# Performance work log

Hardware: AMD Instinct MI355X
Metric: run time of the kernel (lower is better)

The kernel has to match this reference:

```python
import jax, jax.numpy as jnp
import numpy as np

N_POINTS = 200000   # number of voxels
N_CLUSTS = 4096     # number of clusters
P = 64              # points per cluster (regularized fixed size)
E = 32768           # number of (directed) edges


def setup_inputs() -> dict:
    key = jax.random.key(0)
    k1, k2, k3 = jax.random.split(key, 3)
    data = jax.random.normal(k1, (N_POINTS, 4), dtype=jnp.float32)
    clusts = jax.random.randint(k2, (N_CLUSTS, P), 0, N_POINTS, dtype=jnp.int64)
    edge_index = jax.random.randint(k3, (2, E), 0, N_CLUSTS, dtype=jnp.int64)
    return {"data": data, "clusts": clusts, "edge_index": edge_index}


def reference(data, clusts, edge_index):
    coords = data[:, 1:4]                      # [N, 3] voxel coordinates
    c1 = clusts[edge_index[0]]                 # [E, P] point indices of source cluster
    c2 = clusts[edge_index[1]]                 # [E, P] point indices of target cluster
    x1 = coords[c1]                            # [E, P, 3]
    x2 = coords[c2]                            # [E, P, 3]
    e, p = c1.shape
    # pairwise squared distances per edge: [E, P, P]
    d2 = jnp.sum((x1[:, :, None, :] - x2[:, None, :, :]) ** 2, axis=-1)
    imin = jnp.argmin(d2.reshape(e, p * p), axis=1)   # flat argmin of closest pair
    i1 = imin // p
    i2 = imin % p
    v1 = jnp.take_along_axis(x1, i1[:, None, None], axis=1)[:, 0, :]  # [E, 3]
    v2 = jnp.take_along_axis(x2, i2[:, None, None], axis=1)[:, 0, :]  # [E, 3]
    disp = v1 - v2                                                    # [E, 3]
    lend = jnp.linalg.norm(disp, axis=1, keepdims=True)               # [E, 1]
    safe = jnp.where(lend > 0, lend, jnp.ones_like(lend))
    disp = jnp.where(lend > 0, disp / safe, disp)                     # unit displacement
    B = (disp[:, :, None] * disp[:, None, :]).reshape(e, 9)           # outer product, flat
    return jnp.concatenate([v1, v2, disp, lend, B], axis=1)           # [E, 19]
```

## Files before the change

### kernel.cpp

```cpp
#include <hip/hip_runtime.h>

#ifndef FLT_MAX
#define FLT_MAX 3.402823466e+38f
#endif

typedef float v2f __attribute__((ext_vector_type(2)));
typedef float v4f __attribute__((ext_vector_type(4)));
typedef float sf8 __attribute__((ext_vector_type(8)));

__device__ __forceinline__ float rlanef(float v, int l) {
    return __uint_as_float(__builtin_amdgcn_readlane(__float_as_uint(v), l));
}

__device__ __forceinline__ float sel3(int i, float a, float b, float c) {
    return i == 0 ? a : (i == 1 ? b : c);
}

__device__ __forceinline__ float sel4(int i, float a, float b, float c, float d) {
    return i == 0 ? a : (i == 1 ? b : (i == 2 ? c : d));
}

__device__ __forceinline__ float d2f(float ax, float ay, float az,
                                     float bx, float by, float bz) {
    const float dx = __fsub_rn(ax, bx);
    const float dy = __fsub_rn(ay, by);
    const float dz = __fsub_rn(az, bz);
    return __builtin_fmaf(dx, dx, __builtin_fmaf(dy, dy, __fmul_rn(dz, dz)));
}

__device__ __forceinline__ v2f d2p(v2f ax, v2f ay, v2f az, v2f bx, v2f by, v2f bz) {
    const v2f dx = ax - bx, dy = ay - by, dz = az - bz;
    return __builtin_elementwise_fma(dx, dx,
           __builtin_elementwise_fma(dy, dy, dz * dz));
}

__global__ __launch_bounds__(256) void build_table_kernel(
    const float* __restrict__ data,
    const int*   __restrict__ clusts,
    float*       __restrict__ T,
    int C)
{
    const int c = blockIdx.x * 4 + (threadIdx.x >> 6);
    const int p = threadIdx.x & 63;
    if (c >= C) return;
    const int pid = clusts[c * 64 + p];
    const float4 d = *reinterpret_cast<const float4*>(data + (size_t)pid * 4);
    float* row = T + (size_t)c * 192;
    row[p]       = d.y;
    row[p + 64]  = d.z;
    row[p + 128] = d.w;
}

__global__ __launch_bounds__(256) void clustgeo_sload_kernel(
    const float* __restrict__ T,
    const int*   __restrict__ eidx,
    float*       __restrict__ out,
    int E)
{
    const int wave = threadIdx.x >> 6;
    const int lane = threadIdx.x & 63;
    const int e = blockIdx.x * 4 + wave;
    const int ec = e < E ? e : (E - 1);

    const int ca = __builtin_amdgcn_readfirstlane(eidx[ec]);
    const int cb = __builtin_amdgcn_readfirstlane(eidx[E + ec]);
    const float* ta = T + (size_t)ca * 192;
    const float* tb = T + (size_t)cb * 192;

    const float rx = ta[lane];
    const float ry = ta[64 + lane];
    const float rz = ta[128 + lane];
    const v2f rxx = {rx, rx}, ryy = {ry, ry}, rzz = {rz, rz};

    v2f a01 = {FLT_MAX, FLT_MAX};
    v2f a23 = {FLT_MAX, FLT_MAX};

#define COLPAIR(XS, YS, ZS, U, ACC) do {                                       \
    const v2f cx = __builtin_shufflevector(XS, XS, 2*(U), 2*(U)+1);            \
    const v2f cy = __builtin_shufflevector(YS, YS, 2*(U), 2*(U)+1);            \
    const v2f cz = __builtin_shufflevector(ZS, ZS, 2*(U), 2*(U)+1);            \
    ACC = __builtin_elementwise_min(ACC, d2p(rxx, ryy, rzz, cx, cy, cz));      \
} while (0)

#define CHUNK(K) do {                                                          \
    sf8 Xs, Ys, Zs;                                                            \
    asm volatile("s_load_dwordx8 %0, %3, %4\n\t"                               \
                 "s_load_dwordx8 %1, %3, %5\n\t"                               \
                 "s_load_dwordx8 %2, %3, %6\n\t"                               \
                 "s_waitcnt lgkmcnt(0)"                                        \
                 : "=&s"(Xs), "=&s"(Ys), "=&s"(Zs)                             \
                 : "s"(tb), "n"((K) * 32), "n"(256 + (K) * 32),                \
                   "n"(512 + (K) * 32));                                       \
    COLPAIR(Xs, Ys, Zs, 0, a01);                                               \
    COLPAIR(Xs, Ys, Zs, 1, a23);                                               \
    COLPAIR(Xs, Ys, Zs, 2, a01);                                               \
    COLPAIR(Xs, Ys, Zs, 3, a23);                                               \
} while (0)

    CHUNK(0); CHUNK(1); CHUNK(2); CHUNK(3);
    CHUNK(4); CHUNK(5); CHUNK(6); CHUNK(7);
#undef CHUNK
#undef COLPAIR

    const float rowmin = fminf(fminf(a01.x, a01.y), fminf(a23.x, a23.y));

    float bm = rowmin;
    #pragma unroll
    for (int off = 32; off; off >>= 1) bm = fminf(bm, __shfl_xor(bm, off, 64));

    const unsigned long long mi = __ballot(rowmin == bm);
    const int i1 = (int)__ffsll(mi) - 1;
    const float v1x = rlanef(rx, i1);
    const float v1y = rlanef(ry, i1);
    const float v1z = rlanef(rz, i1);

    const float cx2 = tb[lane];
    const float cy2 = tb[64 + lane];
    const float cz2 = tb[128 + lane];
    const float dj = d2f(v1x, v1y, v1z, cx2, cy2, cz2);
    const unsigned long long mj = __ballot(dj == bm);
    const int i2 = (int)__ffsll(mj) - 1;
    const float v2x = rlanef(cx2, i2);
    const float v2y = rlanef(cy2, i2);
    const float v2z = rlanef(cz2, i2);

    float dx = v1x - v2x, dy = v1y - v2y, dz = v1z - v2z;
    const float lend = sqrtf(dx * dx + dy * dy + dz * dz);
    if (lend > 0.f) { dx /= lend; dy /= lend; dz /= lend; }

    if (lane < 19 && e < E) {
        float o;
        if (lane < 3)       o = sel3(lane,     v1x, v1y, v1z);
        else if (lane < 6)  o = sel3(lane - 3, v2x, v2y, v2z);
        else if (lane < 9)  o = sel3(lane - 6, dx, dy, dz);
        else if (lane == 9) o = lend;
        else {
            const int k = lane - 10;
            o = sel3(k / 3, dx, dy, dz) * sel3(k % 3, dx, dy, dz);
        }
        out[(size_t)e * 19 + lane] = o;
    }
}

#define SLICE 196
__global__ __launch_bounds__(256, 4) void clustgeo_edge_fallback(
    const float* __restrict__ data,
    const int*   __restrict__ clusts,
    const int*   __restrict__ eidx,
    float*       __restrict__ out,
    int E)
{
    const int wave = threadIdx.x >> 6;
    const int lane = threadIdx.x & 63;
    const int t    = lane & 15;
    const int gsh  = lane & 48;
    const int e    = blockIdx.x * 16 + wave * 4 + (lane >> 4);
    const int ec   = e < E ? e : (E - 1);

    __shared__ __align__(16) float sx[4][4][SLICE];

    const int ca = eidx[ec];
    const int cb = eidx[E + ec];
    const int4 P1 = *reinterpret_cast<const int4*>(clusts + ca * 64 + 4 * t);
    const int4 P2 = *reinterpret_cast<const int4*>(clusts + cb * 64 + 4 * t);
    const float4 q10 = *reinterpret_cast<const float4*>(data + (size_t)P1.x * 4);
    const float4 q11 = *reinterpret_cast<const float4*>(data + (size_t)P1.y * 4);
    const float4 q12 = *reinterpret_cast<const float4*>(data + (size_t)P1.z * 4);
    const float4 q13 = *reinterpret_cast<const float4*>(data + (size_t)P1.w * 4);
    const float4 q20 = *reinterpret_cast<const float4*>(data + (size_t)P2.x * 4);
    const float4 q21 = *reinterpret_cast<const float4*>(data + (size_t)P2.y * 4);
    const float4 q22 = *reinterpret_cast<const float4*>(data + (size_t)P2.z * 4);
    const float4 q23 = *reinterpret_cast<const float4*>(data + (size_t)P2.w * 4);
    const v4f RX = {q10.y, q11.y, q12.y, q13.y};
    const v4f RY = {q10.z, q11.z, q12.z, q13.z};
    const v4f RZ = {q10.w, q11.w, q12.w, q13.w};
    const v4f CX = {q20.y, q21.y, q22.y, q23.y};
    const v4f CY = {q20.z, q21.z, q22.z, q23.z};
    const v4f CZ = {q20.w, q21.w, q22.w, q23.w};

    float* slice = &sx[wave][lane >> 4][0];
    *reinterpret_cast<v4f*>(slice + 4 * t)       = CX;
    *reinterpret_cast<v4f*>(slice + 64 + 4 * t)  = CY;
    *reinterpret_cast<v4f*>(slice + 128 + 4 * t) = CZ;

    const v4f* SL = reinterpret_cast<const v4f*>(slice);
    v2f a0 = {FLT_MAX, FLT_MAX}, a1 = {FLT_MAX, FLT_MAX};
    v2f a2 = {FLT_MAX, FLT_MAX}, a3 = {FLT_MAX, FLT_MAX};
    #pragma unroll 2
    for (int g = 0; g < 16; ++g) {
        const v4f X = SL[g];
        const v4f Y = SL[16 + g];
        const v4f Z = SL[32 + g];
        const v2f xlo = X.xy, xhi = X.zw, ylo = Y.xy, yhi = Y.zw, zlo = Z.xy, zhi = Z.zw;
        a0 = __builtin_elementwise_min(a0, d2p((v2f){RX.x,RX.x},(v2f){RY.x,RY.x},(v2f){RZ.x,RZ.x}, xlo, ylo, zlo));
        a0 = __builtin_elementwise_min(a0, d2p((v2f){RX.x,RX.x},(v2f){RY.x,RY.x},(v2f){RZ.x,RZ.x}, xhi, yhi, zhi));
        a1 = __builtin_elementwise_min(a1, d2p((v2f){RX.y,RX.y},(v2f){RY.y,RY.y},(v2f){RZ.y,RZ.y}, xlo, ylo, zlo));
        a1 = __builtin_elementwise_min(a1, d2p((v2f){RX.y,RX.y},(v2f){RY.y,RY.y},(v2f){RZ.y,RZ.y}, xhi, yhi, zhi));
        a2 = __builtin_elementwise_min(a2, d2p((v2f){RX.z,RX.z},(v2f){RY.z,RY.z},(v2f){RZ.z,RZ.z}, xlo, ylo, zlo));
        a2 = __builtin_elementwise_min(a2, d2p((v2f){RX.z,RX.z},(v2f){RY.z,RY.z},(v2f){RZ.z,RZ.z}, xhi, yhi, zhi));
        a3 = __builtin_elementwise_min(a3, d2p((v2f){RX.w,RX.w},(v2f){RY.w,RY.w},(v2f){RZ.w,RZ.w}, xlo, ylo, zlo));
        a3 = __builtin_elementwise_min(a3, d2p((v2f){RX.w,RX.w},(v2f){RY.w,RY.w},(v2f){RZ.w,RZ.w}, xhi, yhi, zhi));
    }
    const float m0 = fminf(a0.x, a0.y);
    const float m1 = fminf(a1.x, a1.y);
    const float m2 = fminf(a2.x, a2.y);
    const float m3 = fminf(a3.x, a3.y);
    float bmn = fminf(fminf(m0, m1), fminf(m2, m3));
    #pragma unroll
    for (int off = 8; off; off >>= 1) bmn = fminf(bmn, __shfl_xor(bmn, off, 64));
    const unsigned g0 = (unsigned)(__ballot(m0 == bmn) >> gsh) & 0xFFFFu;
    const unsigned g1 = (unsigned)(__ballot(m1 == bmn) >> gsh) & 0xFFFFu;
    const unsigned g2 = (unsigned)(__ballot(m2 == bmn) >> gsh) & 0xFFFFu;
    const unsigned g3 = (unsigned)(__ballot(m3 == bmn) >> gsh) & 0xFFFFu;
    const int t1 = __builtin_ctz(g0 | g1 | g2 | g3);
    const int s1 = (g0 >> t1) & 1 ? 0 : (g1 >> t1) & 1 ? 1 : (g2 >> t1) & 1 ? 2 : 3;
    const float v1x = __shfl(sel4(s1, RX.x, RX.y, RX.z, RX.w), gsh + t1, 64);
    const float v1y = __shfl(sel4(s1, RY.x, RY.y, RY.z, RY.w), gsh + t1, 64);
    const float v1z = __shfl(sel4(s1, RZ.x, RZ.y, RZ.z, RZ.w), gsh + t1, 64);
    const float d0 = d2f(v1x, v1y, v1z, CX.x, CY.x, CZ.x);
    const float d1 = d2f(v1x, v1y, v1z, CX.y, CY.y, CZ.y);
    const float d2_ = d2f(v1x, v1y, v1z, CX.z, CY.z, CZ.z);
    const float d3 = d2f(v1x, v1y, v1z, CX.w, CY.w, CZ.w);
    const unsigned h0 = (unsigned)(__ballot(d0 == bmn) >> gsh) & 0xFFFFu;
    const unsigned h1 = (unsigned)(__ballot(d1 == bmn) >> gsh) & 0xFFFFu;
    const unsigned h2 = (unsigned)(__ballot(d2_ == bmn) >> gsh) & 0xFFFFu;
    const unsigned h3 = (unsigned)(__ballot(d3 == bmn) >> gsh) & 0xFFFFu;
    const int t2 = __builtin_ctz(h0 | h1 | h2 | h3);
    const int s2 = (h0 >> t2) & 1 ? 0 : (h1 >> t2) & 1 ? 1 : (h2 >> t2) & 1 ? 2 : 3;
    const float v2x = __shfl(sel4(s2, CX.x, CX.y, CX.z, CX.w), gsh + t2, 64);
    const float v2y = __shfl(sel4(s2, CY.x, CY.y, CY.z, CY.w), gsh + t2, 64);
    const float v2z = __shfl(sel4(s2, CZ.x, CZ.y, CZ.z, CZ.w), gsh + t2, 64);
    float dx = v1x - v2x, dy = v1y - v2y, dz = v1z - v2z;
    const float lend = sqrtf(dx * dx + dy * dy + dz * dz);
    if (lend > 0.f) { dx /= lend; dy /= lend; dz /= lend; }
    if (e < E) {
        float* orow = out + (size_t)e * 19;
        float o;
        if (t < 3)       o = sel3(t,     v1x, v1y, v1z);
        else if (t < 6)  o = sel3(t - 3, v2x, v2y, v2z);
        else if (t < 9)  o = sel3(t - 6, dx, dy, dz);
        else if (t == 9) o = lend;
        else {
            const int k = t - 10;
            o = sel3(k / 3, dx, dy, dz) * sel3(k % 3, dx, dy, dz);
        }
        orow[t] = o;
        if (t < 3) {
            const int k = t + 6;
            orow[16 + t] = sel3(k / 3, dx, dy, dz) * sel3(k % 3, dx, dy, dz);
        }
    }
}

extern "C" void kernel_launch(void* const* d_in, const int* in_sizes, int n_in,
                              void* d_out, int out_size, void* d_ws, size_t ws_size,
                              hipStream_t stream) {
    const float* data   = (const float*)d_in[0];
    const int*   clusts = (const int*)d_in[1];
    const int*   eidx   = (const int*)d_in[2];
    float*       out    = (float*)d_out;
    const int E = in_sizes[2] / 2;
    const int C = in_sizes[1] / 64;
    const size_t tbytes = (size_t)C * 192 * sizeof(float);

    if (ws_size >= tbytes) {
        float* T = (float*)d_ws;
        build_table_kernel<<<(C + 3) / 4, 256, 0, stream>>>(data, clusts, T, C);
        clustgeo_sload_kernel<<<(E + 3) / 4, 256, 0, stream>>>(T, eidx, out, E);
    } else {
        clustgeo_edge_fallback<<<(E + 15) / 16, 256, 0, stream>>>(data, clusts, eidx, out, E);
    }
}
```

Baseline: 39.09 us.

## Replace scalar-load column broadcast with DPP row-rotate all-pairs distance scheme

The per-edge 64x64 distance kernel no longer broadcasts target-cluster points via s_load_dwordx8 chunks. Each lane now holds one target point and four source points (one per 16-lane row). The target points rotate within each 16-lane row via DPP row_ror over 16 steps, so the 64x64 pairs are covered without scalar loads or waitcnt stalls. The argmin reduction is reworked to combine across rows with shuffles and to find the source index through per-slot ballots. This adds DPP moves and a more complex index recovery, and tie-breaking must still match the flat argmin order.

```diff
diff --git a/kernel.cpp b/kernel.cpp
--- a/kernel.cpp
+++ b/kernel.cpp
@@ -6,7 +6,6 @@
 
 typedef float v2f __attribute__((ext_vector_type(2)));
 typedef float v4f __attribute__((ext_vector_type(4)));
-typedef float sf8 __attribute__((ext_vector_type(8)));
 
 __device__ __forceinline__ float rlanef(float v, int l) {
     return __uint_as_float(__builtin_amdgcn_readlane(__float_as_uint(v), l));
@@ -18,6 +17,11 @@
 
 __device__ __forceinline__ float sel4(int i, float a, float b, float c, float d) {
     return i == 0 ? a : (i == 1 ? b : (i == 2 ? c : d));
+}
+
+__device__ __forceinline__ float dpp_ror1(float v) {
+    return __int_as_float(__builtin_amdgcn_update_dpp(
+        __float_as_int(v), __float_as_int(v), 0x121, 0xF, 0xF, false));
 }
 
 __device__ __forceinline__ float d2f(float ax, float ay, float az,
@@ -51,7 +55,7 @@
     row[p + 128] = d.w;
 }
 
-__global__ __launch_bounds__(256) void clustgeo_sload_kernel(
+__global__ __launch_bounds__(256) void clustgeo_dpp_kernel(
     const float* __restrict__ T,
     const int*   __restrict__ eidx,
     float*       __restrict__ out,
@@ -59,6 +63,7 @@
 {
     const int wave = threadIdx.x >> 6;
     const int lane = threadIdx.x & 63;
+    const int i    = lane & 15;
     const int e = blockIdx.x * 4 + wave;
     const int ec = e < E ? e : (E - 1);
 
@@ -67,62 +72,69 @@
     const float* ta = T + (size_t)ca * 192;
     const float* tb = T + (size_t)cb * 192;
 
-    const float rx = ta[lane];
-    const float ry = ta[64 + lane];
-    const float rz = ta[128 + lane];
-    const v2f rxx = {rx, rx}, ryy = {ry, ry}, rzz = {rz, rz};
+    const v2f rx01 = {ta[i],       ta[i + 16]};
+    const v2f rx23 = {ta[i + 32],  ta[i + 48]};
+    const v2f ry01 = {ta[64 + i],      ta[64 + i + 16]};
+    const v2f ry23 = {ta[64 + i + 32], ta[64 + i + 48]};
+    const v2f rz01 = {ta[128 + i],      ta[128 + i + 16]};
+    const v2f rz23 = {ta[128 + i + 32], ta[128 + i + 48]};
+
+    float cx = tb[lane];
+    float cy = tb[64 + lane];
+    float cz = tb[128 + lane];
 
     v2f a01 = {FLT_MAX, FLT_MAX};
     v2f a23 = {FLT_MAX, FLT_MAX};
-
-#define COLPAIR(XS, YS, ZS, U, ACC) do {                                       \
-    const v2f cx = __builtin_shufflevector(XS, XS, 2*(U), 2*(U)+1);            \
-    const v2f cy = __builtin_shufflevector(YS, YS, 2*(U), 2*(U)+1);            \
-    const v2f cz = __builtin_shufflevector(ZS, ZS, 2*(U), 2*(U)+1);            \
-    ACC = __builtin_elementwise_min(ACC, d2p(rxx, ryy, rzz, cx, cy, cz));      \
-} while (0)
-
-#define CHUNK(K) do {                                                          \
-    sf8 Xs, Ys, Zs;                                                            \
-    asm volatile("s_load_dwordx8 %0, %3, %4\n\t"                               \
-                 "s_load_dwordx8 %1, %3, %5\n\t"                               \
-                 "s_load_dwordx8 %2, %3, %6\n\t"                               \
-                 "s_waitcnt lgkmcnt(0)"                                        \
-                 : "=&s"(Xs), "=&s"(Ys), "=&s"(Zs)                             \
-                 : "s"(tb), "n"((K) * 32), "n"(256 + (K) * 32),                \
-                   "n"(512 + (K) * 32));                                       \
-    COLPAIR(Xs, Ys, Zs, 0, a01);                                               \
-    COLPAIR(Xs, Ys, Zs, 1, a23);                                               \
-    COLPAIR(Xs, Ys, Zs, 2, a01);                                               \
-    COLPAIR(Xs, Ys, Zs, 3, a23);                                               \
-} while (0)
-
-    CHUNK(0); CHUNK(1); CHUNK(2); CHUNK(3);
-    CHUNK(4); CHUNK(5); CHUNK(6); CHUNK(7);
-#undef CHUNK
-#undef COLPAIR
-
-    const float rowmin = fminf(fminf(a01.x, a01.y), fminf(a23.x, a23.y));
-
-    float bm = rowmin;
     #pragma unroll
-    for (int off = 32; off; off >>= 1) bm = fminf(bm, __shfl_xor(bm, off, 64));
-
-    const unsigned long long mi = __ballot(rowmin == bm);
-    const int i1 = (int)__ffsll(mi) - 1;
-    const float v1x = rlanef(rx, i1);
-    const float v1y = rlanef(ry, i1);
-    const float v1z = rlanef(rz, i1);
-
-    const float cx2 = tb[lane];
-    const float cy2 = tb[64 + lane];
-    const float cz2 = tb[128 + lane];
-    const float dj = d2f(v1x, v1y, v1z, cx2, cy2, cz2);
+    for (int s = 0; s < 16; ++s) {
+        if (s) { cx = dpp_ror1(cx); cy = dpp_ror1(cy); cz = dpp_ror1(cz); }
+        const v2f ccx = {cx, cx};
+        const v2f ccy = {cy, cy};
+        const v2f ccz = {cz, cz};
+        a01 = __builtin_elementwise_min(a01, d2p(rx01, ry01, rz01, ccx, ccy, ccz));
+        a23 = __builtin_elementwise_min(a23, d2p(rx23, ry23, rz23, ccx, ccy, ccz));
+    }
+    cx = dpp_ror1(cx); cy = dpp_ror1(cy); cz = dpp_ror1(cz);
+
+    {
+        v2f t01, t23;
+        t01.x = __shfl_xor(a01.x, 16, 64); t01.y = __shfl_xor(a01.y, 16, 64);
+        t23.x = __shfl_xor(a23.x, 16, 64); t23.y = __shfl_xor(a23.y, 16, 64);
+        a01 = __builtin_elementwise_min(a01, t01);
+        a23 = __builtin_elementwise_min(a23, t23);
+        t01.x = __shfl_xor(a01.x, 32, 64); t01.y = __shfl_xor(a01.y, 32, 64);
+        t23.x = __shfl_xor(a23.x, 32, 64); t23.y = __shfl_xor(a23.y, 32, 64);
+        a01 = __builtin_elementwise_min(a01, t01);
+        a23 = __builtin_elementwise_min(a23, t23);
+    }
+    float bm = fminf(fminf(a01.x, a01.y), fminf(a23.x, a23.y));
+    #pragma unroll
+    for (int off = 8; off; off >>= 1) bm = fminf(bm, __shfl_xor(bm, off, 64));
+
+    const unsigned b0 = (unsigned)__ballot(a01.x == bm) & 0xFFFFu;
+    const unsigned b1 = (unsigned)__ballot(a01.y == bm) & 0xFFFFu;
+    const unsigned b2 = (unsigned)__ballot(a23.x == bm) & 0xFFFFu;
+    const unsigned b3 = (unsigned)__ballot(a23.y == bm) & 0xFFFFu;
+    const int i1 = b0 ? __builtin_ctz(b0)
+                 : b1 ? 16 + __builtin_ctz(b1)
+                 : b2 ? 32 + __builtin_ctz(b2)
+                 :      48 + __builtin_ctz(b3);
+    const int k1 = i1 >> 4;
+    const int ii = i1 & 15;
+
+    const float sxk = sel4(k1, rx01.x, rx01.y, rx23.x, rx23.y);
+    const float syk = sel4(k1, ry01.x, ry01.y, ry23.x, ry23.y);
+    const float szk = sel4(k1, rz01.x, rz01.y, rz23.x, rz23.y);
+    const float v1x = rlanef(sxk, ii);
+    const float v1y = rlanef(syk, ii);
+    const float v1z = rlanef(szk, ii);
+
+    const float dj = d2f(v1x, v1y, v1z, cx, cy, cz);
     const unsigned long long mj = __ballot(dj == bm);
-    const int i2 = (int)__ffsll(mj) - 1;
-    const float v2x = rlanef(cx2, i2);
-    const float v2y = rlanef(cy2, i2);
-    const float v2z = rlanef(cz2, i2);
+    const int j1 = (int)__ffsll(mj) - 1;
+    const float v2x = rlanef(cx, j1);
+    const float v2y = rlanef(cy, j1);
+    const float v2z = rlanef(cz, j1);
 
     float dx = v1x - v2x, dy = v1y - v2y, dz = v1z - v2z;
     const float lend = sqrtf(dx * dx + dy * dy + dz * dz);
@@ -266,7 +278,7 @@
     if (ws_size >= tbytes) {
         float* T = (float*)d_ws;
         build_table_kernel<<<(C + 3) / 4, 256, 0, stream>>>(data, clusts, T, C);
-        clustgeo_sload_kernel<<<(E + 3) / 4, 256, 0, stream>>>(T, eidx, out, E);
+        clustgeo_dpp_kernel<<<(E + 3) / 4, 256, 0, stream>>>(T, eidx, out, E);
     } else {
         clustgeo_edge_fallback<<<(E + 15) / 16, 256, 0, stream>>>(data, clusts, eidx, out, E);
     }
```

Result: slower. 40.04 us (+2.4%).
